# Performance work log

Measured on AMD Instinct MI355X. Metric: run time of the kernel, lower is better.

The kernel has to match this reference:

```python
import jax, jax.numpy as jnp
import numpy as np

# ---- static config matching init_kwargs / input_specs ----
B, H, W_IN, IN_CAPS, ATOMS = 2, 48, 48, 8, 16
KER, STRIDE, OUT_CAPS, ROUTINGS = 3, 1, 16, 3


def setup_inputs() -> dict:
    key = jax.random.key(0)
    k1, k2 = jax.random.split(key)
    x = jax.random.normal(k1, (B, H, W_IN, IN_CAPS * (ATOMS + 1)), dtype=jnp.float32)
    # W: [input_num_capsule, num_capsule, 4, 4], he_normal-ish scale (fan_in=16)
    W = jax.random.normal(k2, (IN_CAPS, OUT_CAPS, 4, 4), dtype=jnp.float32) * np.float32((2.0 / 16.0) ** 0.5)
    return {"input_tensor": x, "W": W}


def _kernel_tile(x, k=KER, stride=STRIDE):
    # Equivalent to the depthwise-conv patch-extraction trick + transpose:
    # output [B, Ho, Wo, k*k, C]
    b, h, w, c = x.shape
    ho = (h - k) // stride + 1
    wo = (w - k) // stride + 1
    patches = jnp.stack(
        [x[:, i:i + stride * ho:stride, j:j + stride * wo:stride, :]
         for i in range(k) for j in range(k)],
        axis=3,
    )
    return patches


def _squash(s, eps=1e-7):
    sq = jnp.sum(s * s, axis=-1, keepdims=True)
    return (sq / (1.0 + sq)) * s / jnp.sqrt(sq + eps)


def reference(input_tensor, W):
    t = _kernel_tile(input_tensor)                      # [B,Ho,Wo,kk,C]
    b, ho, wo, kk, c = t.shape
    n = b * ho * wo
    t = t.reshape(n, kk * IN_CAPS, ATOMS + 1)           # [N, kk*in_caps, 17]
    pose = t[..., :ATOMS].reshape(n, kk, IN_CAPS, 4, 4)
    act = t[..., ATOMS].reshape(n, kk * IN_CAPS)        # input capsule activations
    # vote transform: pose @ W per (input capsule -> output capsule)
    votes = jnp.einsum('nkiab,iobc->nkioac', pose, W)
    votes = votes.reshape(n, kk * IN_CAPS, OUT_CAPS, ATOMS)  # [N, kkin, out, 16]
    # iterative routing-by-agreement, weighted by input activation
    logits = jnp.zeros((n, kk * IN_CAPS, OUT_CAPS), dtype=votes.dtype)
    v = None
    for r in range(ROUTINGS):
        coup = jax.nn.softmax(logits, axis=2) * act[:, :, None]
        s = jnp.einsum('nko,nkoe->noe', coup, votes)    # weighted vote sum
        v = _squash(s)                                  # [N, out, 16]
        if r < ROUTINGS - 1:
            logits = logits + jnp.einsum('nkoe,noe->nko', votes, v)
    return v.reshape(b, ho, wo, OUT_CAPS, ATOMS)
```

## Files before the change

### kernel.cpp

```cpp
#include <hip/hip_runtime.h>


#define IN_CAPS 8
#define OUT_CAPS 16
#define KK 9
#define KKIN 72
#define BATCH 2
#define H_IN 48
#define W_IN 48
#define HO 46
#define WO 46
#define CIN 136
#define NPIX (BATCH*HO*WO)

typedef float v2f __attribute__((ext_vector_type(2)));
typedef float v4f __attribute__((ext_vector_type(4)));

__device__ __forceinline__ v2f lo2(v4f v) { return __builtin_shufflevector(v, v, 0, 1); }
__device__ __forceinline__ v2f hi2(v4f v) { return __builtin_shufflevector(v, v, 2, 3); }
__device__ __forceinline__ v2f fma2(v2f a, v2f b, v2f c) {
    return __builtin_elementwise_fma(a, b, c);
}

template<int CTRL>
__device__ __forceinline__ float dpp_f(float x) {
    return __int_as_float(
        __builtin_amdgcn_update_dpp(0, __float_as_int(x), CTRL, 0xF, 0xF, true));
}
__device__ __forceinline__ float row_sum16(float x) {
    x += dpp_f<0xB1>(x);
    x += dpp_f<0x4E>(x);
    x += dpp_f<0x124>(x);
    x += dpp_f<0x128>(x);
    return x;
}

__device__ __forceinline__ int pose_row(int k) {
    return k * 20 + ((k >> 3) & 1) * 4;
}
__device__ __forceinline__ int g_row(int o, int ic) {
    return (o * 8 + ic) * 20 + o * 4;
}

__global__ __launch_bounds__(256, 2)
void capsule_routing_kernel(const float* __restrict__ x,
                            const float* __restrict__ Wg,
                            float* __restrict__ out)
{
    __shared__ alignas(16) float pose_s[1440];
    __shared__ alignas(16) float pose_t[16 * 76];
    __shared__ float act_s[KKIN];
    __shared__ alignas(16) float g_s[2620];
    __shared__ alignas(16) float coup_s[OUT_CAPS * 76];

    const int tid = threadIdx.x;
    const int o = tid >> 4;
    const int e = tid & 15;
    const int c = e & 3;

    const int n   = blockIdx.x;
    const int b   = n / (HO * WO);
    const int rem = n - b * (HO * WO);
    const int ho  = rem / WO;
    const int wo  = rem - ho * WO;

    v2f w01[IN_CAPS], w23[IN_CAPS];
    #pragma unroll
    for (int i = 0; i < IN_CAPS; ++i) {
        const v4f wv = *reinterpret_cast<const v4f*>(
            &Wg[((i * OUT_CAPS + o) * 4 + c) * 4]);
        w01[i] = lo2(wv);
        w23[i] = hi2(wv);
    }

    for (int idx = tid; idx < KK * CIN; idx += 256) {
        int p  = idx / CIN;
        int cc = idx - p * CIN;
        int py = p / 3, px = p - py * 3;
        float val = x[(((b * H_IN + ho + py) * W_IN) + (wo + px)) * CIN + cc];
        int ic = cc / 17;
        int aa = cc - ic * 17;
        int k  = p * IN_CAPS + ic;
        if (aa == 16) {
            act_s[k] = val;
        } else {
            pose_s[pose_row(k) + aa] = val;
            pose_t[aa * 76 + k] = val;
        }
    }
    __syncthreads();

    if (tid < KKIN) {
        float cv = act_s[tid] * 0.0625f;
        #pragma unroll
        for (int j = 0; j < OUT_CAPS; ++j) coup_s[j * 76 + tid] = cv;
    }

    const v4f* pp = reinterpret_cast<const v4f*>(&pose_t[e * 76]);
    v4f pr[18];
    #pragma unroll
    for (int t = 0; t < 18; ++t) pr[t] = pp[t];

    __syncthreads();

    const int kf  = tid >> 1;
    const int hf  = tid & 1;
    const int ick = kf & 7;
    float lreg8[8] = {0.f,0.f,0.f,0.f,0.f,0.f,0.f,0.f};

    const v4f* cp = reinterpret_cast<const v4f*>(&coup_s[o * 76]);

    float v = 0.f;
    #pragma unroll 1
    for (int r = 0; r < 3; ++r) {
        v2f M01 = {0.f,0.f}, M23 = {0.f,0.f}, M45 = {0.f,0.f}, M67 = {0.f,0.f};
        #pragma unroll
        for (int p = 0; p < KK; ++p) {
            const v4f c0 = cp[2*p], c1 = cp[2*p+1];
            const v4f q0 = pr[2*p], q1 = pr[2*p+1];
            M01 = fma2(lo2(c0), lo2(q0), M01);
            M23 = fma2(hi2(c0), hi2(q0), M23);
            M45 = fma2(lo2(c1), lo2(q1), M45);
            M67 = fma2(hi2(c1), hi2(q1), M67);
        }
        const float Mc[8] = {M01.x, M01.y, M23.x, M23.y,
                             M45.x, M45.y, M67.x, M67.y};
        v2f U01 = {0.f,0.f}, U23 = {0.f,0.f};
        #pragma unroll
        for (int ic = 0; ic < 8; ++ic) {
            const v2f mm = {Mc[ic], Mc[ic]};
            U01 = fma2(w01[ic], mm, U01);
            U23 = fma2(w23[ic], mm, U23);
        }
        float Z0 = U01.x, Z1 = U01.y, Z2 = U23.x, Z3 = U23.y;
        Z0 += dpp_f<0xB1>(Z0); Z1 += dpp_f<0xB1>(Z1);
        Z2 += dpp_f<0xB1>(Z2); Z3 += dpp_f<0xB1>(Z3);
        Z0 += dpp_f<0x4E>(Z0); Z1 += dpp_f<0x4E>(Z1);
        Z2 += dpp_f<0x4E>(Z2); Z3 += dpp_f<0x4E>(Z3);
        const float s = (c == 0) ? Z0 : (c == 1) ? Z1 : (c == 2) ? Z2 : Z3;

        const float sq = row_sum16(s * s);
        v = s * (sq / ((1.f + sq) * sqrtf(sq + 1e-7f)));

        if (r < 2) {
            const float vq0 = dpp_f<0x00>(v);
            const float vq1 = dpp_f<0x55>(v);
            const float vq2 = dpp_f<0xAA>(v);
            const float vq3 = dpp_f<0xFF>(v);
            const v2f vq01 = {vq0, vq1};
            const v2f vq23 = {vq2, vq3};
            #pragma unroll
            for (int ic = 0; ic < 8; ++ic) {
                v2f h = fma2(w23[ic], vq23, w01[ic] * vq01);
                g_s[g_row(o, ic) + e] = h.x + h.y;
            }
            __syncthreads();
            if (tid < 2 * KKIN) {
                const v4f* pk = reinterpret_cast<const v4f*>(
                    &pose_s[pose_row(kf)]);
                const v4f p0 = pk[0], p1 = pk[1], p2 = pk[2], p3 = pk[3];
                const v2f q0 = lo2(p0), q1 = hi2(p0), q2 = lo2(p1), q3 = hi2(p1);
                const v2f q4 = lo2(p2), q5 = hi2(p2), q6 = lo2(p3), q7 = hi2(p3);
                float lg[8];
                #pragma unroll
                for (int j = 0; j < 8; ++j) {
                    const int oo = hf * 8 + j;
                    const v4f* gp = reinterpret_cast<const v4f*>(
                        &g_s[g_row(oo, ick)]);
                    const v4f g0 = gp[0], g1 = gp[1], g2 = gp[2], g3 = gp[3];
                    v2f A  = fma2(q2, lo2(g1), fma2(q4, lo2(g2),
                              fma2(q6, lo2(g3), q0 * lo2(g0))));
                    v2f Bv = fma2(q3, hi2(g1), fma2(q5, hi2(g2),
                              fma2(q7, hi2(g3), q1 * hi2(g0))));
                    lreg8[j] += (A.x + A.y) + (Bv.x + Bv.y);
                    lg[j] = lreg8[j];
                }
                float mx = -1e30f;
                #pragma unroll
                for (int j = 0; j < 8; ++j) mx = fmaxf(mx, lg[j]);
                mx = fmaxf(mx, dpp_f<0xB1>(mx));
                float sum = 0.f;
                #pragma unroll
                for (int j = 0; j < 8; ++j) { lg[j] = __expf(lg[j] - mx); sum += lg[j]; }
                sum += dpp_f<0xB1>(sum);
                const float scale = act_s[kf] / sum;
                #pragma unroll
                for (int j = 0; j < 8; ++j)
                    coup_s[(hf * 8 + j) * 76 + kf] = lg[j] * scale;
            }
            __syncthreads();
        }
    }

    out[n * 256 + tid] = v;
}

extern "C" void kernel_launch(void* const* d_in, const int* in_sizes, int n_in,
                              void* d_out, int out_size, void* d_ws, size_t ws_size,
                              hipStream_t stream) {
    const float* x  = (const float*)d_in[0];
    const float* Wt = (const float*)d_in[1];
    float* outp = (float*)d_out;
    capsule_routing_kernel<<<dim3(NPIX), dim3(256), 0, stream>>>(x, Wt, outp);
}
```

Before: 94.09 us.

## Spread logit update and softmax across all 256 threads with DPP row reductions

The agreement/logit update and softmax were done by 144 threads, each handling 8 output capsules serially. The work is now remapped so every thread owns one output capsule (lane e) for up to 5 input capsules, and the softmax max and sum over the 16 output capsules use DPP row reductions. The per-thread g values are loaded once per iteration and pose offsets and activations are hoisted before the loop. This trades more DPP cross-lane operations and scattered coup_s writes for using all lanes and a shorter serial chain per thread.

```diff
diff --git a/kernel.cpp b/kernel.cpp
--- a/kernel.cpp
+++ b/kernel.cpp
@@ -34,6 +34,13 @@
     x += dpp_f<0x128>(x);
     return x;
 }
+__device__ __forceinline__ float row_max16(float x) {
+    x = fmaxf(x, dpp_f<0xB1>(x));
+    x = fmaxf(x, dpp_f<0x4E>(x));
+    x = fmaxf(x, dpp_f<0x124>(x));
+    x = fmaxf(x, dpp_f<0x128>(x));
+    return x;
+}
 
 __device__ __forceinline__ int pose_row(int k) {
     return k * 20 + ((k >> 3) & 1) * 4;
@@ -49,7 +56,7 @@
 {
     __shared__ alignas(16) float pose_s[1440];
     __shared__ alignas(16) float pose_t[16 * 76];
-    __shared__ float act_s[KKIN];
+    __shared__ alignas(16) float act_s[80];
     __shared__ alignas(16) float g_s[2620];
     __shared__ alignas(16) float coup_s[OUT_CAPS * 76];
 
@@ -101,12 +108,20 @@
     #pragma unroll
     for (int t = 0; t < 18; ++t) pr[t] = pp[t];
 
+    const int icf  = o & 7;
+    const int goff = g_row(e, icf);
+    float act5[5];
+    int   poff5[5];
+    #pragma unroll
+    for (int j = 0; j < 5; ++j) {
+        const int k  = o + 16 * j;
+        const int kk = (k < KKIN) ? k : 0;
+        act5[j]  = act_s[kk];
+        poff5[j] = pose_row(kk);
+    }
+    float lregP[5] = {0.f, 0.f, 0.f, 0.f, 0.f};
+
     __syncthreads();
-
-    const int kf  = tid >> 1;
-    const int hf  = tid & 1;
-    const int ick = kf & 7;
-    float lreg8[8] = {0.f,0.f,0.f,0.f,0.f,0.f,0.f,0.f};
 
     const v4f* cp = reinterpret_cast<const v4f*>(&coup_s[o * 76]);
 
@@ -155,38 +170,23 @@
                 g_s[g_row(o, ic) + e] = h.x + h.y;
             }
             __syncthreads();
-            if (tid < 2 * KKIN) {
-                const v4f* pk = reinterpret_cast<const v4f*>(
-                    &pose_s[pose_row(kf)]);
-                const v4f p0 = pk[0], p1 = pk[1], p2 = pk[2], p3 = pk[3];
-                const v2f q0 = lo2(p0), q1 = hi2(p0), q2 = lo2(p1), q3 = hi2(p1);
-                const v2f q4 = lo2(p2), q5 = hi2(p2), q6 = lo2(p3), q7 = hi2(p3);
-                float lg[8];
-                #pragma unroll
-                for (int j = 0; j < 8; ++j) {
-                    const int oo = hf * 8 + j;
-                    const v4f* gp = reinterpret_cast<const v4f*>(
-                        &g_s[g_row(oo, ick)]);
-                    const v4f g0 = gp[0], g1 = gp[1], g2 = gp[2], g3 = gp[3];
-                    v2f A  = fma2(q2, lo2(g1), fma2(q4, lo2(g2),
-                              fma2(q6, lo2(g3), q0 * lo2(g0))));
-                    v2f Bv = fma2(q3, hi2(g1), fma2(q5, hi2(g2),
-                              fma2(q7, hi2(g3), q1 * hi2(g0))));
-                    lreg8[j] += (A.x + A.y) + (Bv.x + Bv.y);
-                    lg[j] = lreg8[j];
+            const v4f* gp = reinterpret_cast<const v4f*>(&g_s[goff]);
+            const v4f g0 = gp[0], g1 = gp[1], g2 = gp[2], g3 = gp[3];
+            #pragma unroll
+            for (int j = 0; j < 5; ++j) {
+                if (j < 4 || o < 8) {
+                    const v4f* pk = reinterpret_cast<const v4f*>(&pose_s[poff5[j]]);
+                    const v4f p0 = pk[0], p1 = pk[1], p2 = pk[2], p3 = pk[3];
+                    v2f A  = fma2(lo2(p1), lo2(g1), fma2(lo2(p2), lo2(g2),
+                              fma2(lo2(p3), lo2(g3), lo2(p0) * lo2(g0))));
+                    v2f Bv = fma2(hi2(p1), hi2(g1), fma2(hi2(p2), hi2(g2),
+                              fma2(hi2(p3), hi2(g3), hi2(p0) * hi2(g0))));
+                    lregP[j] += (A.x + A.y) + (Bv.x + Bv.y);
+                    const float mx = row_max16(lregP[j]);
+                    const float ex = __expf(lregP[j] - mx);
+                    const float sm = row_sum16(ex);
+                    coup_s[e * 76 + (o + 16 * j)] = ex * (act5[j] / sm);
                 }
-                float mx = -1e30f;
-                #pragma unroll
-                for (int j = 0; j < 8; ++j) mx = fmaxf(mx, lg[j]);
-                mx = fmaxf(mx, dpp_f<0xB1>(mx));
-                float sum = 0.f;
-                #pragma unroll
-                for (int j = 0; j < 8; ++j) { lg[j] = __expf(lg[j] - mx); sum += lg[j]; }
-                sum += dpp_f<0xB1>(sum);
-                const float scale = act_s[kf] / sum;
-                #pragma unroll
-                for (int j = 0; j < 8; ++j)
-                    coup_s[(hf * 8 + j) * 76 + kf] = lg[j] * scale;
             }
             __syncthreads();
         }
```

Result: slower. 96.47 us (+2.5%).
